# Kernel tuning notes

Hardware: AMD Instinct MI355X
Metric: run time of the kernel (lower is better)

Reference implementation:

```python
import jax, jax.numpy as jnp
import numpy as np

N_NODES = 100000
N_EDGES = 3200000
IN_CH = 128
OUT_CH = 64


def gcn_conv(x, src, dst, W, b, n):
    """PyG GCNConv: out = D^{-1/2} (A+I) D^{-1/2} (x @ W) + b.
    src/dst already include self-loops. Aggregation at dst (source_to_target)."""
    deg = jax.ops.segment_sum(jnp.ones_like(dst, x.dtype), dst, num_segments=n)  # [N]
    dinv = jnp.where(deg > 0, jax.lax.rsqrt(deg), 0.0)
    norm = dinv[src] * dinv[dst]                     # [E+N]
    xw = x @ W                                       # [N, out] dense GEMM first (PyG order)
    msgs = xw[src] * norm[:, None]                   # gather + scale, [E+N, out]
    return jax.ops.segment_sum(msgs, dst, num_segments=n) + b


def setup_inputs() -> dict:
    key = jax.random.key(0)
    ks = jax.random.split(key, 6)
    x = jax.random.normal(ks[0], (N_NODES, IN_CH), dtype=jnp.float32)
    edge_index = jax.random.randint(ks[1], (2, N_EDGES), 0, N_NODES, dtype=jnp.int32)
    # Glorot-style init for GCNConv weights
    W1 = jax.random.normal(ks[2], (IN_CH, IN_CH), dtype=jnp.float32) * (1.0 / np.sqrt(IN_CH))
    b1 = jnp.zeros((IN_CH,), dtype=jnp.float32)
    W2 = jax.random.normal(ks[3], (IN_CH, OUT_CH), dtype=jnp.float32) * (1.0 / np.sqrt(IN_CH))
    b2 = jnp.zeros((OUT_CH,), dtype=jnp.float32)
    return {"x": x, "edge_index": edge_index, "W1": W1, "b1": b1, "W2": W2, "b2": b2}


def reference(x, edge_index, W1, b1, W2, b2):
    n = x.shape[0]
    loop = jnp.arange(n, dtype=edge_index.dtype)
    src = jnp.concatenate([edge_index[0], loop])  # add self-loops once; reused by both layers
    dst = jnp.concatenate([edge_index[1], loop])
    h = jax.nn.sigmoid(gcn_conv(x, src, dst, W1, b1, n))
    return jax.nn.sigmoid(gcn_conv(h, src, dst, W2, b2, n))
```

## Files before the change

### kernel.cpp

```cpp
#include <hip/hip_runtime.h>
#include <hip/hip_bf16.h>
#include <hip/hip_fp16.h>

#define IN_CH 128
#define NODES_PER_BUCKET 128
#define BUCKET_CAP 5120
#define EPB 8192

using f32x2 = __attribute__((ext_vector_type(2))) float;

__device__ __forceinline__ float sigmoidf_(float x) { return 1.0f / (1.0f + __expf(-x)); }
__device__ __forceinline__ __half2 u2h(unsigned u) { return __builtin_bit_cast(__half2, u); }
__device__ __forceinline__ unsigned packh2(float a, float b) {
    return __builtin_bit_cast(unsigned, __float22half2_rn(make_float2(a, b)));
}

#if __has_builtin(__builtin_amdgcn_cvt_pk_f32_fp8) && __has_builtin(__builtin_amdgcn_cvt_pk_fp8_f32)
#define FP8_HW 1
#else
#define FP8_HW 0
__device__ __forceinline__ unsigned fp8_enc1(float f) {
    unsigned short us = __builtin_bit_cast(unsigned short, __float2half(f));
    unsigned s = (us >> 8) & 0x80u;
    unsigned mag = us & 0x7fffu;
    if (mag < 0x2400u) return s;
    unsigned t = mag - 0x2000u;
    t += 0x3Fu + ((t >> 7) & 1u);
    unsigned r = t >> 7;
    if (r > 0x7Eu) r = 0x7Eu;
    return s | r;
}
__device__ __forceinline__ float fp8_dec1(unsigned v) {
    unsigned s = (v & 0x80u) << 8;
    unsigned m = v & 0x7Fu;
    unsigned h = m ? (((m << 7) + 0x2000u) | s) : s;
    return __half2float(__builtin_bit_cast(__half, (unsigned short)h));
}
#endif

__device__ __forceinline__ void acc16(float* a, uint4 v) {
#if FP8_HW
    f32x2 t;
    t = __builtin_amdgcn_cvt_pk_f32_fp8(v.x, false); a[0] += t[0];  a[1] += t[1];
    t = __builtin_amdgcn_cvt_pk_f32_fp8(v.x, true);  a[2] += t[0];  a[3] += t[1];
    t = __builtin_amdgcn_cvt_pk_f32_fp8(v.y, false); a[4] += t[0];  a[5] += t[1];
    t = __builtin_amdgcn_cvt_pk_f32_fp8(v.y, true);  a[6] += t[0];  a[7] += t[1];
    t = __builtin_amdgcn_cvt_pk_f32_fp8(v.z, false); a[8] += t[0];  a[9] += t[1];
    t = __builtin_amdgcn_cvt_pk_f32_fp8(v.z, true);  a[10] += t[0]; a[11] += t[1];
    t = __builtin_amdgcn_cvt_pk_f32_fp8(v.w, false); a[12] += t[0]; a[13] += t[1];
    t = __builtin_amdgcn_cvt_pk_f32_fp8(v.w, true);  a[14] += t[0]; a[15] += t[1];
#else
    unsigned d[4] = {v.x, v.y, v.z, v.w};
#pragma unroll
    for (int q = 0; q < 4; q++)
#pragma unroll
        for (int b = 0; b < 4; b++) a[q * 4 + b] += fp8_dec1((d[q] >> (8 * b)) & 0xffu);
#endif
}

__device__ __forceinline__ unsigned pack4fp8(float a, float b, float c, float d) {
#if FP8_HW
    unsigned r = 0;
    r = __builtin_amdgcn_cvt_pk_fp8_f32(a, b, r, false);
    r = __builtin_amdgcn_cvt_pk_fp8_f32(c, d, r, true);
    return r;
#else
    return fp8_enc1(a) | (fp8_enc1(b) << 8) | (fp8_enc1(c) << 16) | (fp8_enc1(d) << 24);
#endif
}

__global__ __launch_bounds__(256) void k_bucket_scatter(const int* __restrict__ src,
                                                        const int* __restrict__ dst, int E,
                                                        int* __restrict__ bucketCnt, int NB,
                                                        unsigned* __restrict__ pairBuf) {
    __shared__ int hist[1024];
    int tid = threadIdx.x;
    for (int t = tid; t < 1024; t += 256) hist[t] = 0;
    __syncthreads();
    int base = blockIdx.x * EPB;
    int end = min(base + EPB, E);
    int cnt = end - base;
    int cnt4 = cnt >> 2;
    const int4* d4 = (const int4*)(dst + base);
    const int4* s4 = (const int4*)(src + base);

    unsigned pr[8][4];
    unsigned rkb[8][4];
#pragma unroll
    for (int j = 0; j < 8; j++) {
        int i = tid + j * 256;
        if (i < cnt4) {
            int4 d = d4[i];
            int4 s = s4[i];
            int b, r;
            b = d.x >> 7; r = atomicAdd(&hist[b], 1);
            pr[j][0] = ((unsigned)s.x << 7) | (unsigned)(d.x & 127); rkb[j][0] = ((unsigned)r << 10) | (unsigned)b;
            b = d.y >> 7; r = atomicAdd(&hist[b], 1);
            pr[j][1] = ((unsigned)s.y << 7) | (unsigned)(d.y & 127); rkb[j][1] = ((unsigned)r << 10) | (unsigned)b;
            b = d.z >> 7; r = atomicAdd(&hist[b], 1);
            pr[j][2] = ((unsigned)s.z << 7) | (unsigned)(d.z & 127); rkb[j][2] = ((unsigned)r << 10) | (unsigned)b;
            b = d.w >> 7; r = atomicAdd(&hist[b], 1);
            pr[j][3] = ((unsigned)s.w << 7) | (unsigned)(d.w & 127); rkb[j][3] = ((unsigned)r << 10) | (unsigned)b;
        }
    }
    unsigned prT = 0, rkbT = 0;
    bool hasT = false;
    {
        int tl = cnt & 3;
        if (tid < tl) {
            int i = base + (cnt4 << 2) + tid;
            int d = dst[i];
            int b = d >> 7;
            int r = atomicAdd(&hist[b], 1);
            prT = ((unsigned)src[i] << 7) | (unsigned)(d & 127);
            rkbT = ((unsigned)r << 10) | (unsigned)b;
            hasT = true;
        }
    }
    __syncthreads();
    for (int t = tid; t < NB; t += 256) {
        int c = hist[t];
        hist[t] = c ? atomicAdd(&bucketCnt[t], c) : 0;
    }
    __syncthreads();
#pragma unroll
    for (int j = 0; j < 8; j++) {
        int i = tid + j * 256;
        if (i < cnt4) {
#pragma unroll
            for (int q = 0; q < 4; q++) {
                unsigned t = rkb[j][q];
                int b = (int)(t & 1023u);
                int pos = hist[b] + (int)(t >> 10);
                if (pos < BUCKET_CAP) pairBuf[(size_t)b * BUCKET_CAP + pos] = pr[j][q];
            }
        }
    }
    if (hasT) {
        int b = (int)(rkbT & 1023u);
        int pos = hist[b] + (int)(rkbT >> 10);
        if (pos < BUCKET_CAP) pairBuf[(size_t)b * BUCKET_CAP + pos] = prT;
    }
}

__global__ __launch_bounds__(1024) void k_scan_buckets(const int* __restrict__ bucketCnt, int NB,
                                                       int* __restrict__ bucketBase,
                                                       int* __restrict__ rowptr, int n) {
    __shared__ int sh[1024];
    int t = threadIdx.x;
    int v = (t < NB) ? min(bucketCnt[t], BUCKET_CAP) : 0;
    sh[t] = v;
    __syncthreads();
    for (int off = 1; off < 1024; off <<= 1) {
        int u = (t >= off) ? sh[t - off] : 0;
        __syncthreads();
        sh[t] += u;
        __syncthreads();
    }
    if (t < NB) bucketBase[t] = sh[t] - v;
    if (t == 1023) rowptr[n] = sh[1023];
}

__global__ __launch_bounds__(256) void k_bucket_place2(const unsigned* __restrict__ pairBuf,
                                                       const int* __restrict__ bucketCnt,
                                                       const int* __restrict__ bucketBase,
                                                       int* __restrict__ rowptr,
                                                       float* __restrict__ dinv,
                                                       int* __restrict__ col, int n) {
    __shared__ int hist[NODES_PER_BUCKET];
    __shared__ int excl[NODES_PER_BUCKET];
    __shared__ int stage[BUCKET_CAP];
    int b = blockIdx.x;
    int tid = threadIdx.x;
    int first = b * NODES_PER_BUCKET;
    if (tid < NODES_PER_BUCKET) hist[tid] = 0;
    __syncthreads();
    int cb = min(bucketCnt[b], BUCKET_CAP);
    const unsigned* p = pairBuf + (size_t)b * BUCKET_CAP;
    for (int e = tid; e < cb; e += 256) atomicAdd(&hist[p[e] & 127], 1);
    __syncthreads();
    int v = (tid < NODES_PER_BUCKET) ? hist[tid] : 0;
    if (tid < NODES_PER_BUCKET) excl[tid] = v;
    __syncthreads();
    for (int off = 1; off < NODES_PER_BUCKET; off <<= 1) {
        int u = (tid < NODES_PER_BUCKET && tid >= off) ? excl[tid - off] : 0;
        __syncthreads();
        if (tid < NODES_PER_BUCKET) excl[tid] += u;
        __syncthreads();
    }
    int base = bucketBase[b];
    if (tid < NODES_PER_BUCKET) {
        int node = first + tid;
        int ex = excl[tid] - v;
        if (node < n) {
            rowptr[node] = base + ex;
            dinv[node] = rsqrtf((float)(v + 1));
        }
        hist[tid] = ex;
    }
    __syncthreads();
    for (int e = tid; e < cb; e += 256) {
        unsigned pr = p[e];
        int lpos = atomicAdd(&hist[pr & 127], 1);
        stage[lpos] = (int)(pr >> 7);
    }
    __syncthreads();
    for (int i = tid; i < cb; i += 256) col[base + i] = stage[i];
}

template <int OUTC, bool INHALF>
__global__ __launch_bounds__(256) void k_gemm_scale(const void* __restrict__ Xv,
                                                    const float* __restrict__ W,
                                                    const float* __restrict__ dinv,
                                                    unsigned char* __restrict__ Yb, int n) {
    constexpr int TN = OUTC / 16;
    __shared__ float xs[16][65];
    __shared__ float ws[16 * OUTC];
    int tid = threadIdx.x;
    int row0 = blockIdx.x * 64;
    int tx = tid & 15;
    int ty = tid >> 4;

    float acc[4][TN];
#pragma unroll
    for (int i = 0; i < 4; i++)
#pragma unroll
        for (int j = 0; j < TN; j++) acc[i][j] = 0.0f;

    for (int k0 = 0; k0 < IN_CH; k0 += 16) {
        {
            int r = tid >> 2;
            int kq = (tid & 3) * 4;
            int grow = row0 + r;
            float4 xv = make_float4(0.f, 0.f, 0.f, 0.f);
            if (grow < n) {
                if constexpr (INHALF) {
                    uint2 xu = *(const uint2*)((const unsigned short*)Xv + (size_t)grow * IN_CH + k0 + kq);
                    __half2 p0 = u2h(xu.x), p1 = u2h(xu.y);
                    xv = make_float4(__low2float(p0), __high2float(p0), __low2float(p1), __high2float(p1));
                } else {
                    xv = *(const float4*)((const float*)Xv + (size_t)grow * IN_CH + k0 + kq);
                }
            }
            xs[kq + 0][r] = xv.x;
            xs[kq + 1][r] = xv.y;
            xs[kq + 2][r] = xv.z;
            xs[kq + 3][r] = xv.w;
        }
        {
            const float4* wsrc = (const float4*)(W + k0 * OUTC);
            float4* wdst = (float4*)ws;
#pragma unroll
            for (int j = 0; j < OUTC / 64; j++) wdst[tid + j * 256] = wsrc[tid + j * 256];
        }
        __syncthreads();
#pragma unroll
        for (int kk = 0; kk < 16; kk++) {
            float a[4];
            *(float4*)a = *(const float4*)&xs[kk][ty * 4];
            float bb[TN];
#pragma unroll
            for (int j = 0; j < TN / 4; j++)
                *(float4*)&bb[j * 4] = *(const float4*)&ws[kk * OUTC + tx * TN + j * 4];
#pragma unroll
            for (int i = 0; i < 4; i++)
#pragma unroll
                for (int j = 0; j < TN; j++) acc[i][j] = fmaf(a[i], bb[j], acc[i][j]);
        }
        __syncthreads();
    }
#pragma unroll
    for (int i = 0; i < 4; i++) {
        int grow = row0 + ty * 4 + i;
        if (grow < n) {
            float dvv = dinv[grow];
            if constexpr (TN == 8) {
                uint2 o;
                o.x = pack4fp8(acc[i][0] * dvv, acc[i][1] * dvv, acc[i][2] * dvv, acc[i][3] * dvv);
                o.y = pack4fp8(acc[i][4] * dvv, acc[i][5] * dvv, acc[i][6] * dvv, acc[i][7] * dvv);
                ((uint2*)(Yb + (size_t)grow * 128))[tx] = o;
            } else {
                unsigned o = pack4fp8(acc[i][0] * dvv, acc[i][1] * dvv, acc[i][2] * dvv, acc[i][3] * dvv);
                ((unsigned*)(Yb + (size_t)grow * 64))[tx] = o;
            }
        }
    }
}

template <int C, bool OUTHALF>
__global__ __launch_bounds__(256) void k_agg(const uint4* __restrict__ Y4,
                                             const int* __restrict__ rowptr,
                                             const int* __restrict__ col,
                                             const float* __restrict__ dinv,
                                             const float* __restrict__ bias,
                                             void* __restrict__ out, int n, int zidx) {
    constexpr int LPE = C / 16;
    constexpr int NPW = 64 / LPE;
    constexpr int RS = C / 16;
    int gid = blockIdx.x * blockDim.x + threadIdx.x;
    int wid = gid >> 6;
    int lane = gid & 63;
    int g = lane / LPE;
    int sub = lane % LPE;
    int node = wid * NPW + g;
    bool valid = node < n;
    int nc = valid ? node : 0;
    int s0 = rowptr[nc];
    int s1 = valid ? rowptr[nc + 1] : s0;

    float a0[16];
#pragma unroll
    for (int k = 0; k < 16; k++) a0[k] = 0.f;

    {
        int idx = valid ? node : zidx;
        uint4 v = Y4[(size_t)idx * RS + sub];
        acc16(a0, v);
    }
    int e = s0;
    for (; e + 8 <= s1; e += 8) {
        int c0 = col[e];
        int c1 = col[e + 1];
        int c2 = col[e + 2];
        int c3 = col[e + 3];
        int c4 = col[e + 4];
        int c5 = col[e + 5];
        int c6 = col[e + 6];
        int c7 = col[e + 7];
        uint4 v0 = Y4[(size_t)c0 * RS + sub];
        uint4 v1 = Y4[(size_t)c1 * RS + sub];
        uint4 v2 = Y4[(size_t)c2 * RS + sub];
        uint4 v3 = Y4[(size_t)c3 * RS + sub];
        uint4 v4 = Y4[(size_t)c4 * RS + sub];
        uint4 v5 = Y4[(size_t)c5 * RS + sub];
        uint4 v6 = Y4[(size_t)c6 * RS + sub];
        uint4 v7 = Y4[(size_t)c7 * RS + sub];
        acc16(a0, v0);
        acc16(a0, v1);
        acc16(a0, v2);
        acc16(a0, v3);
        acc16(a0, v4);
        acc16(a0, v5);
        acc16(a0, v6);
        acc16(a0, v7);
    }
    if (e < s1) {
        int i0 = min(e + 0, s1 - 1), i1 = min(e + 1, s1 - 1);
        int i2 = min(e + 2, s1 - 1), i3 = min(e + 3, s1 - 1);
        int i4 = min(e + 4, s1 - 1), i5 = min(e + 5, s1 - 1);
        int i6 = min(e + 6, s1 - 1), i7 = min(e + 7, s1 - 1);
        int c0 = (e + 0 < s1) ? col[i0] : zidx;
        int c1 = (e + 1 < s1) ? col[i1] : zidx;
        int c2 = (e + 2 < s1) ? col[i2] : zidx;
        int c3 = (e + 3 < s1) ? col[i3] : zidx;
        int c4 = (e + 4 < s1) ? col[i4] : zidx;
        int c5 = (e + 5 < s1) ? col[i5] : zidx;
        int c6 = (e + 6 < s1) ? col[i6] : zidx;
        int c7 = (e + 7 < s1) ? col[i7] : zidx;
        uint4 v0 = Y4[(size_t)c0 * RS + sub];
        uint4 v1 = Y4[(size_t)c1 * RS + sub];
        uint4 v2 = Y4[(size_t)c2 * RS + sub];
        uint4 v3 = Y4[(size_t)c3 * RS + sub];
        uint4 v4 = Y4[(size_t)c4 * RS + sub];
        uint4 v5 = Y4[(size_t)c5 * RS + sub];
        uint4 v6 = Y4[(size_t)c6 * RS + sub];
        uint4 v7 = Y4[(size_t)c7 * RS + sub];
        acc16(a0, v0);
        acc16(a0, v1);
        acc16(a0, v2);
        acc16(a0, v3);
        acc16(a0, v4);
        acc16(a0, v5);
        acc16(a0, v6);
        acc16(a0, v7);
    }

    if (valid) {
        float dv = dinv[node];
        float4 bv[4];
        bv[0] = *(const float4*)&bias[sub * 16];
        bv[1] = *(const float4*)&bias[sub * 16 + 4];
        bv[2] = *(const float4*)&bias[sub * 16 + 8];
        bv[3] = *(const float4*)&bias[sub * 16 + 12];
        float o[16];
#pragma unroll
        for (int q = 0; q < 4; q++) {
            const float* bq = (const float*)&bv[q];
#pragma unroll
            for (int b = 0; b < 4; b++) o[q * 4 + b] = sigmoidf_(a0[q * 4 + b] * dv + bq[b]);
        }
        if constexpr (OUTHALF) {
            constexpr int OR = C / 8;
            uint4 h0, h1;
            h0.x = packh2(o[0], o[1]);   h0.y = packh2(o[2], o[3]);
            h0.z = packh2(o[4], o[5]);   h0.w = packh2(o[6], o[7]);
            h1.x = packh2(o[8], o[9]);   h1.y = packh2(o[10], o[11]);
            h1.z = packh2(o[12], o[13]); h1.w = packh2(o[14], o[15]);
            ((uint4*)out)[(size_t)node * OR + sub * 2] = h0;
            ((uint4*)out)[(size_t)node * OR + sub * 2 + 1] = h1;
        } else {
            float* op = (float*)out + (size_t)node * C + sub * 16;
            *(float4*)(op + 0)  = make_float4(o[0], o[1], o[2], o[3]);
            *(float4*)(op + 4)  = make_float4(o[4], o[5], o[6], o[7]);
            *(float4*)(op + 8)  = make_float4(o[8], o[9], o[10], o[11]);
            *(float4*)(op + 12) = make_float4(o[12], o[13], o[14], o[15]);
        }
    }
}

extern "C" void kernel_launch(void* const* d_in, const int* in_sizes, int n_in,
                              void* d_out, int out_size, void* d_ws, size_t ws_size,
                              hipStream_t stream) {
    const float* x  = (const float*)d_in[0];
    const int* eidx = (const int*)d_in[1];
    const float* W1 = (const float*)d_in[2];
    const float* b1 = (const float*)d_in[3];
    const float* W2 = (const float*)d_in[4];
    const float* b2 = (const float*)d_in[5];
    float* out = (float*)d_out;

    int n = in_sizes[0] / IN_CH;
    int E = in_sizes[1] / 2;
    const int* srcv = eidx;
    const int* dstv = eidx + E;
    int NB = (n + NODES_PER_BUCKET - 1) / NODES_PER_BUCKET;

    char* w = (char*)d_ws;
    auto alloc = [&](size_t bytes) {
        char* p = w;
        w += (bytes + 255) & ~(size_t)255;
        return p;
    };
    int* bucketCnt      = (int*)alloc((size_t)NB * 4);
    int* bucketBase     = (int*)alloc((size_t)NB * 4);
    unsigned* pairBuf   = (unsigned*)alloc((size_t)NB * BUCKET_CAP * 4);
    int* rowptr         = (int*)alloc(((size_t)n + 1) * 4);
    float* dinv         = (float*)alloc((size_t)n * 4);
    int* col            = (int*)alloc((size_t)E * 4);
    unsigned char* y    = (unsigned char*)alloc(((size_t)n + 1) * 128);
    unsigned short* h   = (unsigned short*)alloc((size_t)n * IN_CH * 2);

    hipMemsetAsync(bucketCnt, 0, (size_t)NB * 4, stream);
    hipMemsetAsync(y + (size_t)n * 128, 0, 128, stream);

    int nblk = (E + EPB - 1) / EPB;
    k_bucket_scatter<<<nblk, 256, 0, stream>>>(srcv, dstv, E, bucketCnt, NB, pairBuf);
    k_scan_buckets<<<1, 1024, 0, stream>>>(bucketCnt, NB, bucketBase, rowptr, n);
    k_bucket_place2<<<NB, 256, 0, stream>>>(pairBuf, bucketCnt, bucketBase, rowptr, dinv, col, n);

    int gemmGrid = (n + 63) / 64;

    k_gemm_scale<128, false><<<gemmGrid, 256, 0, stream>>>(x, W1, dinv, y, n);
    k_agg<128, true><<<(n + 31) / 32, 256, 0, stream>>>((const uint4*)y, rowptr, col, dinv, b1, h, n, n);
    k_gemm_scale<64, true><<<gemmGrid, 256, 0, stream>>>(h, W2, dinv, y, n);
    k_agg<64, false><<<(n + 63) / 64, 256, 0, stream>>>((const uint4*)y, rowptr, col, dinv, b2, out, n, 2 * n);
}
```

Measured before the change: 241.2 us.

## Replace FP32 SIMT GEMM with FP16 MFMA and pre-transposed half weights

Swaps the shared-memory FP32 FMA GEMM for a kernel using 16x16x32 FP16 MFMA instructions. Each wave computes 16 rows and reads its X rows and the weight fragments directly from global memory. A small prep kernel transposes W1 and W2 and converts them to FP16 so the fragment loads are contiguous. This removes LDS staging and scalar FMA cost. In exchange it adds FP16 rounding of the layer-1 input and weights, plus one extra tiny launch.

Measured after the change: 222.0 us, median of 2. -8.0%, faster.

```diff
diff --git a/kernel.cpp b/kernel.cpp
--- a/kernel.cpp
+++ b/kernel.cpp
@@ -8,6 +8,8 @@
 #define EPB 8192
 
 using f32x2 = __attribute__((ext_vector_type(2))) float;
+using f32x4 = __attribute__((ext_vector_type(4))) float;
+using f16x8 = __attribute__((ext_vector_type(8))) _Float16;
 
 __device__ __forceinline__ float sigmoidf_(float x) { return 1.0f / (1.0f + __expf(-x)); }
 __device__ __forceinline__ __half2 u2h(unsigned u) { return __builtin_bit_cast(__half2, u); }
@@ -208,81 +210,68 @@
     for (int i = tid; i < cb; i += 256) col[base + i] = stage[i];
 }
 
+__global__ __launch_bounds__(256) void k_wprep(const float* __restrict__ W1,
+                                               const float* __restrict__ W2,
+                                               _Float16* __restrict__ wT1,
+                                               _Float16* __restrict__ wT2) {
+    int i = blockIdx.x * 256 + threadIdx.x;
+    if (i < 128 * 128) {
+        int nn = i >> 7, k = i & 127;
+        wT1[i] = (_Float16)W1[k * 128 + nn];
+    }
+    if (i < 64 * 128) {
+        int nn = i >> 7, k = i & 127;
+        wT2[i] = (_Float16)W2[k * 64 + nn];
+    }
+}
+
 template <int OUTC, bool INHALF>
-__global__ __launch_bounds__(256) void k_gemm_scale(const void* __restrict__ Xv,
-                                                    const float* __restrict__ W,
-                                                    const float* __restrict__ dinv,
-                                                    unsigned char* __restrict__ Yb, int n) {
-    constexpr int TN = OUTC / 16;
-    __shared__ float xs[16][65];
-    __shared__ float ws[16 * OUTC];
+__global__ __launch_bounds__(256) void k_gemm_mfma(const void* __restrict__ Xv,
+                                                   const _Float16* __restrict__ wT,
+                                                   const float* __restrict__ dinv,
+                                                   unsigned char* __restrict__ Yb, int n) {
+    constexpr int NT = OUTC / 16;
     int tid = threadIdx.x;
-    int row0 = blockIdx.x * 64;
-    int tx = tid & 15;
-    int ty = tid >> 4;
-
-    float acc[4][TN];
-#pragma unroll
-    for (int i = 0; i < 4; i++)
-#pragma unroll
-        for (int j = 0; j < TN; j++) acc[i][j] = 0.0f;
-
-    for (int k0 = 0; k0 < IN_CH; k0 += 16) {
-        {
-            int r = tid >> 2;
-            int kq = (tid & 3) * 4;
-            int grow = row0 + r;
-            float4 xv = make_float4(0.f, 0.f, 0.f, 0.f);
-            if (grow < n) {
-                if constexpr (INHALF) {
-                    uint2 xu = *(const uint2*)((const unsigned short*)Xv + (size_t)grow * IN_CH + k0 + kq);
-                    __half2 p0 = u2h(xu.x), p1 = u2h(xu.y);
-                    xv = make_float4(__low2float(p0), __high2float(p0), __low2float(p1), __high2float(p1));
-                } else {
-                    xv = *(const float4*)((const float*)Xv + (size_t)grow * IN_CH + k0 + kq);
-                }
-            }
-            xs[kq + 0][r] = xv.x;
-            xs[kq + 1][r] = xv.y;
-            xs[kq + 2][r] = xv.z;
-            xs[kq + 3][r] = xv.w;
-        }
-        {
-            const float4* wsrc = (const float4*)(W + k0 * OUTC);
-            float4* wdst = (float4*)ws;
-#pragma unroll
-            for (int j = 0; j < OUTC / 64; j++) wdst[tid + j * 256] = wsrc[tid + j * 256];
-        }
-        __syncthreads();
-#pragma unroll
-        for (int kk = 0; kk < 16; kk++) {
-            float a[4];
-            *(float4*)a = *(const float4*)&xs[kk][ty * 4];
-            float bb[TN];
-#pragma unroll
-            for (int j = 0; j < TN / 4; j++)
-                *(float4*)&bb[j * 4] = *(const float4*)&ws[kk * OUTC + tx * TN + j * 4];
-#pragma unroll
-            for (int i = 0; i < 4; i++)
-#pragma unroll
-                for (int j = 0; j < TN; j++) acc[i][j] = fmaf(a[i], bb[j], acc[i][j]);
-        }
-        __syncthreads();
-    }
-#pragma unroll
-    for (int i = 0; i < 4; i++) {
-        int grow = row0 + ty * 4 + i;
-        if (grow < n) {
-            float dvv = dinv[grow];
-            if constexpr (TN == 8) {
-                uint2 o;
-                o.x = pack4fp8(acc[i][0] * dvv, acc[i][1] * dvv, acc[i][2] * dvv, acc[i][3] * dvv);
-                o.y = pack4fp8(acc[i][4] * dvv, acc[i][5] * dvv, acc[i][6] * dvv, acc[i][7] * dvv);
-                ((uint2*)(Yb + (size_t)grow * 128))[tx] = o;
-            } else {
-                unsigned o = pack4fp8(acc[i][0] * dvv, acc[i][1] * dvv, acc[i][2] * dvv, acc[i][3] * dvv);
-                ((unsigned*)(Yb + (size_t)grow * 64))[tx] = o;
-            }
+    int wave = tid >> 6;
+    int lane = tid & 63;
+    int tx = lane & 15;
+    int q = lane >> 4;
+    int r0 = blockIdx.x * 64 + wave * 16;
+    int m = r0 + tx;
+    int mc = min(m, n - 1);
+
+    f32x4 acc[NT];
+#pragma unroll
+    for (int nt = 0; nt < NT; nt++) acc[nt] = (f32x4)(0.0f);
+
+#pragma unroll
+    for (int ks = 0; ks < 4; ks++) {
+        int k0 = ks * 32 + q * 8;
+        f16x8 bfrag;
+        if constexpr (INHALF) {
+            bfrag = *(const f16x8*)((const _Float16*)Xv + (size_t)mc * 128 + k0);
+        } else {
+            const float* xr = (const float*)Xv + (size_t)mc * 128 + k0;
+            float4 x0 = *(const float4*)xr;
+            float4 x1 = *(const float4*)(xr + 4);
+            bfrag[0] = (_Float16)x0.x; bfrag[1] = (_Float16)x0.y;
+            bfrag[2] = (_Float16)x0.z; bfrag[3] = (_Float16)x0.w;
+            bfrag[4] = (_Float16)x1.x; bfrag[5] = (_Float16)x1.y;
+            bfrag[6] = (_Float16)x1.z; bfrag[7] = (_Float16)x1.w;
+        }
+#pragma unroll
+        for (int nt = 0; nt < NT; nt++) {
+            f16x8 afrag = *(const f16x8*)(wT + (size_t)(nt * 16 + tx) * 128 + k0);
+            acc[nt] = __builtin_amdgcn_mfma_f32_16x16x32_f16(afrag, bfrag, acc[nt], 0, 0, 0);
+        }
+    }
+    if (m < n) {
+        float dv = dinv[m];
+        unsigned char* yrow = Yb + (size_t)m * OUTC;
+#pragma unroll
+        for (int nt = 0; nt < NT; nt++) {
+            unsigned d = pack4fp8(acc[nt][0] * dv, acc[nt][1] * dv, acc[nt][2] * dv, acc[nt][3] * dv);
+            *(unsigned*)(yrow + nt * 16 + q * 4) = d;
         }
     }
 }
@@ -439,10 +428,13 @@
     int* col            = (int*)alloc((size_t)E * 4);
     unsigned char* y    = (unsigned char*)alloc(((size_t)n + 1) * 128);
     unsigned short* h   = (unsigned short*)alloc((size_t)n * IN_CH * 2);
+    _Float16* wT1       = (_Float16*)alloc(128 * 128 * 2);
+    _Float16* wT2       = (_Float16*)alloc(64 * 128 * 2);
 
     hipMemsetAsync(bucketCnt, 0, (size_t)NB * 4, stream);
     hipMemsetAsync(y + (size_t)n * 128, 0, 128, stream);
 
+    k_wprep<<<64, 256, 0, stream>>>(W1, W2, wT1, wT2);
     int nblk = (E + EPB - 1) / EPB;
     k_bucket_scatter<<<nblk, 256, 0, stream>>>(srcv, dstv, E, bucketCnt, NB, pairBuf);
     k_scan_buckets<<<1, 1024, 0, stream>>>(bucketCnt, NB, bucketBase, rowptr, n);
@@ -450,8 +442,8 @@
 
     int gemmGrid = (n + 63) / 64;
 
-    k_gemm_scale<128, false><<<gemmGrid, 256, 0, stream>>>(x, W1, dinv, y, n);
+    k_gemm_mfma<128, false><<<gemmGrid, 256, 0, stream>>>(x, wT1, dinv, y, n);
     k_agg<128, true><<<(n + 31) / 32, 256, 0, stream>>>((const uint4*)y, rowptr, col, dinv, b1, h, n, n);
-    k_gemm_scale<64, true><<<gemmGrid, 256, 0, stream>>>(h, W2, dinv, y, n);
+    k_gemm_mfma<64, true><<<gemmGrid, 256, 0, stream>>>(h, wT2, dinv, y, n);
     k_agg<64, false><<<(n + 63) / 64, 256, 0, stream>>>((const uint4*)y, rowptr, col, dinv, b2, out, n, 2 * n);
 }
```
